# Kernel optimization log

Hardware: AMD Instinct MI355X
Metric: run time of the kernel (lower is better)

## Reference

```python
import jax, jax.numpy as jnp
import numpy as np
from jax import lax

DIM = 192
NUM_CLASSES = 4
D_INNER = 2 * DIM          # expand=2
D_STATE = 16
D_CONV = 4
DT_RANK = (DIM + 15) // 16  # ceil(192/16)=12
PATCH = 16


def _mamba_params(key, prefix):
    ks = jax.random.split(key, 9)
    s = lambda k, shape, scale: (jax.random.normal(k, shape, jnp.float32) * scale)
    p = {
        prefix + '_in_w':   s(ks[0], (2 * D_INNER, DIM), 0.02),
        prefix + '_conv_w': s(ks[1], (D_INNER, D_CONV), 0.1),
        prefix + '_conv_b': jnp.zeros((D_INNER,), jnp.float32),
        prefix + '_xproj_w': s(ks[2], (DT_RANK + 2 * D_STATE, D_INNER), 0.02),
        prefix + '_dt_w':   s(ks[3], (D_INNER, DT_RANK), 0.1),
        prefix + '_dt_b':   s(ks[4], (D_INNER,), 0.1),
        # A_log init: log(1..d_state) broadcast over d_inner (mamba default)
        prefix + '_A_log':  jnp.broadcast_to(jnp.log(jnp.arange(1, D_STATE + 1, dtype=jnp.float32)), (D_INNER, D_STATE)) + 0.0,
        prefix + '_D':      jnp.ones((D_INNER,), jnp.float32),
        prefix + '_out_w':  s(ks[5], (DIM, D_INNER), 0.02),
    }
    return p


def setup_inputs() -> dict:
    key = jax.random.key(0)
    ks = jax.random.split(key, 8)
    inp = {
        'x': jax.random.normal(ks[0], (32, 3, 384, 384), jnp.float32),
        'patch_w': jax.random.normal(ks[1], (DIM, 3, PATCH, PATCH), jnp.float32) * 0.02,
        'patch_b': jnp.zeros((DIM,), jnp.float32),
        'ln_g': jnp.ones((DIM,), jnp.float32),
        'ln_b': jnp.zeros((DIM,), jnp.float32),
        'fc_w': jax.random.normal(ks[2], (NUM_CLASSES, DIM), jnp.float32) * 0.02,
        'fc_b': jnp.zeros((NUM_CLASSES,), jnp.float32),
    }
    inp.update(_mamba_params(ks[3], 'f'))
    inp.update(_mamba_params(ks[4], 'b'))
    return inp


def _layernorm(x, g, b, eps=1e-5):
    mu = jnp.mean(x, -1, keepdims=True)
    var = jnp.mean(jnp.square(x - mu), -1, keepdims=True)
    return (x - mu) * lax.rsqrt(var + eps) * g + b


def _mamba(x, in_w, conv_w, conv_b, xproj_w, dt_w, dt_b, A_log, Dskip, out_w):
    # x: [B, L, DIM]
    Bn, L, _ = x.shape
    xz = x @ in_w.T                                    # [B, L, 2*di]
    xi, z = jnp.split(xz, 2, axis=-1)
    # causal depthwise conv1d, kernel D_CONV, left pad
    xp = jnp.pad(xi, ((0, 0), (D_CONV - 1, 0), (0, 0)))
    xc = conv_b + sum(xp[:, k:k + L, :] * conv_w[:, k] for k in range(D_CONV))
    xc = jax.nn.silu(xc)                               # [B, L, di]
    proj = xc @ xproj_w.T                              # [B, L, dtr+2*ds]
    dt, Bm, Cm = jnp.split(proj, [DT_RANK, DT_RANK + D_STATE], axis=-1)
    dt = jax.nn.softplus(dt @ dt_w.T + dt_b)           # [B, L, di]
    A = -jnp.exp(A_log)                                # [di, ds]

    def step(h, inp):
        dt_t, B_t, C_t, x_t = inp                      # [B,di],[B,ds],[B,ds],[B,di]
        dA = jnp.exp(dt_t[:, :, None] * A)             # [B, di, ds]
        h = dA * h + (dt_t * x_t)[:, :, None] * B_t[:, None, :]
        y = jnp.einsum('bds,bs->bd', h, C_t)
        return h, y

    h0 = jnp.zeros((Bn, D_INNER, D_STATE), x.dtype)
    xs = (dt.transpose(1, 0, 2), Bm.transpose(1, 0, 2),
          Cm.transpose(1, 0, 2), xc.transpose(1, 0, 2))
    _, ys = lax.scan(step, h0, xs)                     # [L, B, di]
    y = ys.transpose(1, 0, 2) + xc * Dskip
    y = y * jax.nn.silu(z)
    return y @ out_w.T                                 # [B, L, DIM]


def reference(x, patch_w, patch_b, ln_g, ln_b, fc_w, fc_b,
              f_in_w, f_conv_w, f_conv_b, f_xproj_w, f_dt_w, f_dt_b, f_A_log, f_D, f_out_w,
              b_in_w, b_conv_w, b_conv_b, b_xproj_w, b_dt_w, b_dt_b, b_A_log, b_D, b_out_w):
    Bn, C, H, W = x.shape
    Hp, Wp = H // PATCH, W // PATCH
    # patch embed: stride==kernel conv == reshape + einsum
    xr = x.reshape(Bn, C, Hp, PATCH, Wp, PATCH)
    tok = jnp.einsum('bchpwq,dcpq->bhwd', xr, patch_w) + patch_b
    tok = tok.reshape(Bn, Hp * Wp, DIM)                # [B, L, D]
    tok = _layernorm(tok, ln_g, ln_b)
    fwd = _mamba(tok, f_in_w, f_conv_w, f_conv_b, f_xproj_w, f_dt_w, f_dt_b, f_A_log, f_D, f_out_w)
    bwd = _mamba(tok[:, ::-1, :], b_in_w, b_conv_w, b_conv_b, b_xproj_w, b_dt_w, b_dt_b, b_A_log, b_D, b_out_w)
    out = fwd + bwd[:, ::-1, :]
    pooled = jnp.mean(out, axis=1)                     # adaptive avg pool to 1
    return pooled @ fc_w.T + fc_b                      # [B, num_classes]
```

## Files before the change

### kernel.cpp

```cpp
#include <hip/hip_runtime.h>
#include <hip/hip_bf16.h>

#define NC 32
#define CL 18

typedef __attribute__((ext_vector_type(8))) short short8;
typedef __attribute__((ext_vector_type(4))) float f32x4;
typedef __attribute__((ext_vector_type(2))) float f32x2;

__device__ __forceinline__ float sigm(float x){ return 1.0f/(1.0f+__expf(-x)); }

__device__ __forceinline__ ushort f2bf(float f){
  unsigned u = __float_as_uint(f);
  unsigned r = (u + 0x7fffu + ((u>>16)&1u)) >> 16;
  return (ushort)r;
}
__device__ __forceinline__ float bf2f(ushort h){ return __uint_as_float(((unsigned)h)<<16); }

__global__ __launch_bounds__(256) void k_prep_all(
    const float* __restrict__ patch_w, const float* __restrict__ f_in_w,
    const float* __restrict__ b_in_w,
    const float* __restrict__ f_xw, const float* __restrict__ b_xw,
    const float* __restrict__ f_cw, const float* __restrict__ b_cw,
    const float* __restrict__ f_al, const float* __restrict__ b_al,
    const float* __restrict__ fc_w, const float* __restrict__ f_ow,
    const float* __restrict__ b_ow,
    ushort* __restrict__ pw_h, ushort* __restrict__ pw_l,
    ushort* __restrict__ iw_h, ushort* __restrict__ iw_l,
    ushort* __restrict__ xw_h, ushort* __restrict__ xw_l,
    float* __restrict__ cwT, float* __restrict__ Abuf,
    float* __restrict__ A0fl, float* __restrict__ W2){
  const int bx = blockIdx.x, t = threadIdx.x;
  if (bx < 1728){
    int which = bx/576;
    int i = (bx - which*576)*256 + t;
    if (which==0){
      float f = patch_w[i];
      ushort hb = f2bf(f);
      pw_h[i]=hb; pw_l[i]=f2bf(f - bf2f(hb));
    } else {
      const float* src = (which==1) ? f_in_w : b_in_w;
      int dirofs = (which==1) ? 0 : 48;
      float f = src[i];
      int n = i/192, k = i%192;
      int nblk = n>>4, r = n&15, kblk = k>>5, kk = k&31;
      int lane = r + ((kk>>3)<<4), j = kk&7;
      size_t idx = ((size_t)((nblk+dirofs)*6 + kblk)*64 + lane)*8 + j;
      ushort hb = f2bf(f);
      iw_h[idx]=hb; iw_l[idx]=f2bf(f - bf2f(hb));
    }
  } else if (bx < 1872){
    int i = (bx-1728)*256 + t;
    int dir=i/(48*384), rem=i%(48*384), n=rem/384, k=rem%384;
    float v = (n<44) ? (dir?b_xw:f_xw)[n*384+k] : 0.f;
    ushort hb = f2bf(v);
    xw_h[i]=hb; xw_l[i]=f2bf(v - bf2f(hb));
  } else if (bx < 1884){
    int i = (bx-1872)*256 + t;
    int dir=i/1536, rem=i%1536, j=rem/384, k=rem%384;
    cwT[i] = (dir ? b_cw : f_cw)[k*4+j];
  } else if (bx < 1887){
    int i = (bx-1884)*256 + t;
    if (i < 768){
      int dir=i/384, di=i%384;
      const float* alp = (dir?b_al:f_al) + di*16;
      float A0 = -expf(alp[0]);
      bool fast = true;
      Abuf[(size_t)i*16] = A0;
      #pragma unroll
      for (int s=1;s<16;s++){
        float A = -expf(alp[s]);
        Abuf[(size_t)i*16+s] = A;
        fast = fast && (fabsf(A - (s+1)*A0) <= 1e-5f*(s+1)*fabsf(A0));
      }
      A0fl[i*2]=A0; A0fl[i*2+1]=fast?1.f:0.f;
    }
  } else {
    int i = (bx-1887)*256 + t;
    if (i < 768){
      int dir=i/384, di=i%384;
      const float* ow = dir ? b_ow : f_ow;
      float a0=0.f,a1=0.f,a2=0.f,a3=0.f;
      for (int d=0; d<192; ++d){
        float o = ow[d*384 + di];
        a0 += fc_w[0*192+d]*o; a1 += fc_w[1*192+d]*o;
        a2 += fc_w[2*192+d]*o; a3 += fc_w[3*192+d]*o;
      }
      W2[(0*2+dir)*384+di]=a0; W2[(1*2+dir)*384+di]=a1;
      W2[(2*2+dir)*384+di]=a2; W2[(3*2+dir)*384+di]=a3;
    }
  }
}
__device__ __forceinline__ float w2at(const float* W2, int dir, int ch, int di){
  return W2[(ch*2+dir)*384+di];
}

__global__ __launch_bounds__(1024) void k_patch(
    const float* __restrict__ x,
    const ushort* __restrict__ pw_h, const ushort* __restrict__ pw_l,
    const float* __restrict__ pb, const float* __restrict__ lng,
    const float* __restrict__ lnb,
    ushort* __restrict__ tokf_h, ushort* __restrict__ tokf_l,
    int b0, int Mc){
  __shared__ __align__(16) char sBmem[49152];
  __shared__ __align__(16) ushort sAh[64*64], sAl[64*64];
  __shared__ float sLN[4][64][2];
  ushort* sBh = (ushort*)sBmem;
  ushort* sBl = (ushort*)(sBmem + 24576);
  const int tid = threadIdx.x;
  const int m0 = blockIdx.x*64;
  const int lane = tid&63, w = tid>>6;
  const int wr = w>>2, wc = w&3;
  const int r = lane&15, g = lane>>4;
  f32x4 acc[3];
  #pragma unroll
  for (int i=0;i<3;i++) acc[i] = (f32x4){0.f,0.f,0.f,0.f};

  for (int s=0;s<12;s++){
    const int c = s>>2, p0 = (s&3)*4;
    {
      int f = tid;
      int m = f>>4, rem = f&15, pp = rem>>2, qq = rem&3;
      int rm = m0 + m;
      float4 v = make_float4(0.f,0.f,0.f,0.f);
      if (rm < Mc){
        int b = b0 + rm/576, l = rm%576, hp = l/24, wp = l%24;
        size_t idx4 = ((size_t)((b*3+c)*384) + hp*16 + p0+pp)*96 + wp*4 + qq;
        v = reinterpret_cast<const float4*>(x)[idx4];
      }
      ushort4 hv, lv;
      hv.x=f2bf(v.x); lv.x=f2bf(v.x-bf2f(hv.x));
      hv.y=f2bf(v.y); lv.y=f2bf(v.y-bf2f(hv.y));
      hv.z=f2bf(v.z); lv.z=f2bf(v.z-bf2f(hv.z));
      hv.w=f2bf(v.w); lv.w=f2bf(v.w-bf2f(hv.w));
      int byte = (m*128 + pp*32 + qq*8) ^ ((m&7)<<4);
      *reinterpret_cast<ushort4*>((char*)sAh + byte) = hv;
      *reinterpret_cast<ushort4*>((char*)sAl + byte) = lv;
    }
    #pragma unroll
    for (int i=0;i<2;i++){
      int f = tid + i*1024;
      if (f < 1536){
        int n = f>>3, k8 = f&7;
        size_t gi = (size_t)n*768 + s*64 + k8*8;
        uint4 bh = *reinterpret_cast<const uint4*>(pw_h + gi);
        uint4 bl = *reinterpret_cast<const uint4*>(pw_l + gi);
        int byte = (n*128 + k8*16) ^ ((n&7)<<4);
        *reinterpret_cast<uint4*>((char*)sBh + byte) = bh;
        *reinterpret_cast<uint4*>((char*)sBl + byte) = bl;
      }
    }
    __syncthreads();
    #pragma unroll
    for (int kk=0;kk<2;kk++){
      int arow = wr*16 + r;
      int abyte = (arow*128 + kk*64 + g*16) ^ ((arow&7)<<4);
      short8 ah = *reinterpret_cast<const short8*>((char*)sAh + abyte);
      short8 al = *reinterpret_cast<const short8*>((char*)sAl + abyte);
      #pragma unroll
      for (int nfl=0; nfl<3; nfl++){
        int brow = (wc*3+nfl)*16 + r;
        int bbyte = (brow*128 + kk*64 + g*16) ^ ((brow&7)<<4);
        short8 bh = *reinterpret_cast<const short8*>((char*)sBh + bbyte);
        short8 bll = *reinterpret_cast<const short8*>((char*)sBl + bbyte);
        acc[nfl] = __builtin_amdgcn_mfma_f32_16x16x32_bf16(ah, bh, acc[nfl], 0,0,0);
        acc[nfl] = __builtin_amdgcn_mfma_f32_16x16x32_bf16(ah, bll, acc[nfl], 0,0,0);
        acc[nfl] = __builtin_amdgcn_mfma_f32_16x16x32_bf16(al, bh, acc[nfl], 0,0,0);
      }
    }
    __syncthreads();
  }
  float pbv[3], gv[3], bv[3];
  #pragma unroll
  for (int nfl=0;nfl<3;nfl++){
    int col = (wc*3+nfl)*16 + r;
    pbv[nfl]=pb[col]; gv[nfl]=lng[col]; bv[nfl]=lnb[col];
  }
  #pragma unroll
  for (int nfl=0;nfl<3;nfl++)
    #pragma unroll
    for (int q=0;q<4;q++) acc[nfl][q] += pbv[nfl];
  float sum[4]={0,0,0,0}, sq[4]={0,0,0,0};
  #pragma unroll
  for (int nfl=0;nfl<3;nfl++)
    #pragma unroll
    for (int q=0;q<4;q++){ float v=acc[nfl][q]; sum[q]+=v; sq[q]+=v*v; }
  #pragma unroll
  for (int off=1; off<16; off<<=1){
    #pragma unroll
    for (int q=0;q<4;q++){
      sum[q]+=__shfl_xor(sum[q],off);
      sq[q] +=__shfl_xor(sq[q],off);
    }
  }
  if (r==0){
    #pragma unroll
    for (int q=0;q<4;q++){
      int row = wr*16 + g*4 + q;
      sLN[wc][row][0]=sum[q]; sLN[wc][row][1]=sq[q];
    }
  }
  __syncthreads();
  float* sT = (float*)sBmem;
  #pragma unroll
  for (int q=0;q<4;q++){
    int rl = wr*16 + g*4 + q;
    float stot = sLN[0][rl][0]+sLN[1][rl][0]+sLN[2][rl][0]+sLN[3][rl][0];
    float qtot = sLN[0][rl][1]+sLN[1][rl][1]+sLN[2][rl][1]+sLN[3][rl][1];
    float mu = stot*(1.f/192.f);
    float var = qtot*(1.f/192.f) - mu*mu;
    float rs = rsqrtf(var + 1e-5f);
    #pragma unroll
    for (int nfl=0;nfl<3;nfl++)
      sT[rl*192 + (wc*3+nfl)*16 + r] = (acc[nfl][q]-mu)*rs*gv[nfl] + bv[nfl];
  }
  __syncthreads();
  const int mB = m0>>4;
  #pragma unroll
  for (int i=0;i<2;i++){
    int fl = tid + 1024*i;
    if (fl < 1536){
      int mb = fl/384, rem = fl-mb*384, kb = rem>>6, ln = rem&63;
      int rr = ln&15, gq = ln>>4;
      const float* sp = sT + (mb*16+rr)*192 + kb*32 + gq*8;
      short8 hv, lv;
      #pragma unroll
      for (int j=0;j<8;j++){
        float v = sp[j];
        ushort hb = f2bf(v);
        hv[j] = (short)hb;
        lv[j] = (short)f2bf(v - bf2f(hb));
      }
      size_t o = ((size_t)((mB+mb)*6 + kb)*64 + ln)*8;
      *reinterpret_cast<short8*>(tokf_h + o) = hv;
      *reinterpret_cast<short8*>(tokf_l + o) = lv;
    }
  }
}

__global__ __launch_bounds__(1024) void k_inproj(
    const ushort* __restrict__ tokf_h, const ushort* __restrict__ tokf_l,
    const ushort* __restrict__ iw_h, const ushort* __restrict__ iw_l,
    float* __restrict__ xib, ushort* __restrict__ zb, int Bc, int Mc){
  __shared__ __align__(16) char sMem[65536];
  ushort* sAh = (ushort*)sMem;
  ushort* sAl = (ushort*)(sMem + 16384);
  ushort* sBh = (ushort*)(sMem + 32768);
  ushort* sBl = (ushort*)(sMem + 49152);
  const int tid = threadIdx.x;
  const int lane = tid&63, w = tid>>6;
  const int wr = w>>2, wc = w&3;
  const int r = lane&15, g = lane>>4;
  const int m0 = blockIdx.x*128;
  const int mb0 = blockIdx.x*8;
  const int nb0 = blockIdx.y*8;
  const int n0d = (blockIdx.y%6)*128;
  const bool dir1 = (blockIdx.y >= 6);
  const bool isZ = ((blockIdx.y%6) >= 3);

  f32x4 acc[2][2];
  #pragma unroll
  for (int a=0;a<2;a++)
    #pragma unroll
    for (int b=0;b<2;b++) acc[a][b] = (f32x4){0.f,0.f,0.f,0.f};

  for (int s=0;s<3;s++){
    {
      const int f = w;
      const int mf = f>>1, kk = f&1;
      const size_t ga = ((size_t)((mb0+mf)*6 + 2*s+kk)*64 + lane)*8;
      const size_t gb = ((size_t)((nb0+mf)*6 + 2*s+kk)*64 + lane)*8;
      const int so = f*512 + lane*8;
      *reinterpret_cast<short8*>(sAh+so) = *reinterpret_cast<const short8*>(tokf_h+ga);
      *reinterpret_cast<short8*>(sBh+so) = *reinterpret_cast<const short8*>(iw_h+gb);
      if (!isZ){
        *reinterpret_cast<short8*>(sAl+so) = *reinterpret_cast<const short8*>(tokf_l+ga);
        *reinterpret_cast<short8*>(sBl+so) = *reinterpret_cast<const short8*>(iw_l+gb);
      }
    }
    __syncthreads();
    #pragma unroll
    for (int kk=0;kk<2;kk++){
      short8 ah[2], al[2];
      #pragma unroll
      for (int mf=0;mf<2;mf++){
        const int fo = ((wr*2+mf)*2+kk)*512 + lane*8;
        ah[mf] = *reinterpret_cast<const short8*>(sAh+fo);
        if (!isZ) al[mf] = *reinterpret_cast<const short8*>(sAl+fo);
      }
      #pragma unroll
      for (int nf=0;nf<2;nf++){
        const int fo = ((wc*2+nf)*2+kk)*512 + lane*8;
        short8 bh = *reinterpret_cast<const short8*>(sBh+fo);
        if (isZ){
          #pragma unroll
          for (int mf=0;mf<2;mf++)
            acc[mf][nf] = __builtin_amdgcn_mfma_f32_16x16x32_bf16(ah[mf], bh, acc[mf][nf], 0,0,0);
        } else {
          short8 bl = *reinterpret_cast<const short8*>(sBl+fo);
          #pragma unroll
          for (int mf=0;mf<2;mf++){
            acc[mf][nf] = __builtin_amdgcn_mfma_f32_16x16x32_bf16(ah[mf], bh, acc[mf][nf], 0,0,0);
            acc[mf][nf] = __builtin_amdgcn_mfma_f32_16x16x32_bf16(ah[mf], bl, acc[mf][nf], 0,0,0);
            acc[mf][nf] = __builtin_amdgcn_mfma_f32_16x16x32_bf16(al[mf], bh, acc[mf][nf], 0,0,0);
          }
        }
      }
    }
    __syncthreads();
  }

  float* sT = reinterpret_cast<float*>(sMem);
  const int h_of_w = wr>>1;
  #pragma unroll
  for (int h=0; h<2; h++){
    if (h==1) __syncthreads();
    if (h_of_w == h){
      #pragma unroll
      for (int mf=0;mf<2;mf++)
        #pragma unroll
        for (int nf=0;nf<2;nf++)
          #pragma unroll
          for (int q=0;q<4;q++){
            int rl = (wr&1)*32 + mf*16 + g*4 + q;
            int c  = wc*32 + nf*16 + r;
            sT[rl*132 + c] = acc[mf][nf][q];
          }
    }
    __syncthreads();
    {
      const int rl = tid>>4, cg = tid&15;
      const int rm = m0 + h*64 + rl;
      if (rm < Mc){
        size_t row;
        if (dir1){
          int bl = rm/576, l = rm - bl*576;
          row = (size_t)(Bc + bl)*576 + (575-l);
        } else {
          row = (size_t)rm;
        }
        const float* sp = sT + rl*132 + cg*8;
        if (!isZ){
          *reinterpret_cast<f32x4*>(xib + row*384 + n0d + cg*8)     = *reinterpret_cast<const f32x4*>(sp);
          *reinterpret_cast<f32x4*>(xib + row*384 + n0d + cg*8 + 4) = *reinterpret_cast<const f32x4*>(sp+4);
        } else {
          short8 hv;
          #pragma unroll
          for (int j=0;j<8;j++){
            float v = sp[j];
            v = v*sigm(v);
            hv[j] = (short)f2bf(v);
          }
          *reinterpret_cast<short8*>(zb + row*384 + (n0d-384) + cg*8) = hv;
        }
      }
    }
  }
}

__global__ __launch_bounds__(256) void k_convx(
    const float* __restrict__ xib, const float* __restrict__ cwT,
    const float* __restrict__ f_cb, const float* __restrict__ b_cb,
    const ushort* __restrict__ xw_h, const ushort* __restrict__ xw_l,
    float* __restrict__ proj, ushort* __restrict__ xcb, int Bc){
  __shared__ __align__(16) float sRaw[67*64];
  __shared__ __align__(16) ushort sAh[64*64], sAl[64*64];
  __shared__ __align__(16) ushort sBh[48*64], sBl[48*64];
  const int dir = blockIdx.z, blk = blockIdx.y, l0 = blockIdx.x*64;
  const int tid = threadIdx.x, lane = tid&63, w = tid>>6;
  const int r = lane&15, g = lane>>4;
  const size_t seq = ((size_t)dir*Bc + blk)*576;
  const float* cwTd = cwT + dir*1536;
  const float* cbp  = dir?b_cb:f_cb;
  const ushort* bhp = xw_h + dir*48*384;
  const ushort* blp = xw_l + dir*48*384;
  f32x4 acc[3];
  #pragma unroll
  for (int i=0;i<3;i++) acc[i] = (f32x4){0.f,0.f,0.f,0.f};

  for (int kc=0; kc<6; ++kc){
    #pragma unroll
    for (int i=0;i<5;i++){
      int f = tid + i*256;
      if (f < 67*16){
        int rr = f>>4, kq = f&15;
        int l = l0 + rr - 3;
        float4 v = make_float4(0.f,0.f,0.f,0.f);
        if (l >= 0) v = *reinterpret_cast<const float4*>(xib + (seq+l)*384 + kc*64 + kq*4);
        int kqs = kq ^ (rr&15);
        *reinterpret_cast<float4*>(sRaw + rr*64 + kqs*4) = v;
      }
    }
    __syncthreads();
    #pragma unroll
    for (int i=0;i<4;i++){
      int f = tid + i*256;
      int m = f>>4, kq = f&15;
      float4 a = reinterpret_cast<const float4*>(cbp)[kc*16 + kq];
      #pragma unroll
      for (int j=0;j<4;j++){
        int rr = m + j;
        float4 rv = *reinterpret_cast<const float4*>(sRaw + rr*64 + (kq ^ (rr&15))*4);
        float4 cv = reinterpret_cast<const float4*>(cwTd)[j*96 + kc*16 + kq];
        a.x += cv.x*rv.x; a.y += cv.y*rv.y; a.z += cv.z*rv.z; a.w += cv.w*rv.w;
      }
      a.x = a.x*sigm(a.x); a.y = a.y*sigm(a.y); a.z = a.z*sigm(a.z); a.w = a.w*sigm(a.w);
      ushort4 hv, lv;
      hv.x=f2bf(a.x); lv.x=f2bf(a.x-bf2f(hv.x));
      hv.y=f2bf(a.y); lv.y=f2bf(a.y-bf2f(hv.y));
      hv.z=f2bf(a.z); lv.z=f2bf(a.z-bf2f(hv.z));
      hv.w=f2bf(a.w); lv.w=f2bf(a.w-bf2f(hv.w));
      *reinterpret_cast<ushort4*>(xcb + (seq + l0 + m)*384 + kc*64 + kq*4) = hv;
      int byte = (m*128 + kq*8) ^ ((m&7)<<4);
      *reinterpret_cast<ushort4*>((char*)sAh + byte) = hv;
      *reinterpret_cast<ushort4*>((char*)sAl + byte) = lv;
    }
    #pragma unroll
    for (int i=0;i<2;i++){
      int f = tid + i*256;
      if (f < 384){
        int n = f>>3, k8 = f&7;
        size_t gi = (size_t)n*384 + kc*64 + k8*8;
        uint4 vh = *reinterpret_cast<const uint4*>(bhp + gi);
        uint4 vl = *reinterpret_cast<const uint4*>(blp + gi);
        int byte = (n*128 + k8*16) ^ ((n&7)<<4);
        *reinterpret_cast<uint4*>((char*)sBh + byte) = vh;
        *reinterpret_cast<uint4*>((char*)sBl + byte) = vl;
      }
    }
    __syncthreads();
    #pragma unroll
    for (int kk=0;kk<2;kk++){
      int arow = w*16 + r;
      int abyte = (arow*128 + kk*64 + g*16) ^ ((arow&7)<<4);
      short8 ah = *reinterpret_cast<const short8*>((char*)sAh + abyte);
      short8 al = *reinterpret_cast<const short8*>((char*)sAl + abyte);
      #pragma unroll
      for (int nf=0;nf<3;nf++){
        int brow = nf*16 + r;
        int bbyte = (brow*128 + kk*64 + g*16) ^ ((brow&7)<<4);
        short8 bh = *reinterpret_cast<const short8*>((char*)sBh + bbyte);
        short8 bll = *reinterpret_cast<const short8*>((char*)sBl + bbyte);
        acc[nf] = __builtin_amdgcn_mfma_f32_16x16x32_bf16(ah, bh, acc[nf], 0,0,0);
        acc[nf] = __builtin_amdgcn_mfma_f32_16x16x32_bf16(ah, bll, acc[nf], 0,0,0);
        acc[nf] = __builtin_amdgcn_mfma_f32_16x16x32_bf16(al, bh, acc[nf], 0,0,0);
      }
    }
    __syncthreads();
  }
  #pragma unroll
  for (int nf=0;nf<3;nf++){
    int col = nf*16 + r;
    if (col < 44){
      #pragma unroll
      for (int q=0;q<4;q++){
        int l = l0 + w*16 + g*4 + q;
        proj[(seq+l)*44 + col] = acc[nf][q];
      }
    }
  }
}

__global__ __launch_bounds__(256) void k_scan_p1(
    const ushort* __restrict__ zb, const ushort* __restrict__ xcb,
    const float* __restrict__ proj,
    const float* __restrict__ f_dtw, const float* __restrict__ b_dtw,
    const float* __restrict__ f_dtb, const float* __restrict__ b_dtb,
    const float* __restrict__ A0fl, const float* __restrict__ Abuf,
    const float* __restrict__ f_D,  const float* __restrict__ b_D,
    const float* __restrict__ W2, float* __restrict__ dtend,
    float* __restrict__ hbuf, float* __restrict__ part, int b0, int Bc){
  const int dir=blockIdx.z, bl=blockIdx.y;
  const int gg=blockIdx.x>>3, cq=blockIdx.x&7;
  const int wv=threadIdx.x>>6, lane=threadIdx.x&63;
  const int c = cq*4 + wv;
  const int di = gg*64 + lane;
  const size_t seq = ((size_t)dir*Bc + bl)*576;
  const float* dtwp = (dir?b_dtw:f_dtw) + di*12;
  float dtw[12];
  #pragma unroll
  for (int i=0;i<3;i++){
    float4 t = reinterpret_cast<const float4*>(dtwp)[i];
    dtw[4*i]=t.x; dtw[4*i+1]=t.y; dtw[4*i+2]=t.z; dtw[4*i+3]=t.w;
  }
  float dtb = (dir?b_dtb:f_dtb)[di];
  float2 af = reinterpret_cast<const float2*>(A0fl)[dir*384+di];
  const float A0 = af.x;
  const bool fast = (af.y != 0.f);
  float A[16];
  if (!fast){
    #pragma unroll
    for (int s=0;s<16;s++) A[s] = Abuf[((size_t)dir*384+di)*16+s];
  }
  float Dv = (dir?b_D:f_D)[di];
  float w2c[4];
  #pragma unroll
  for (int ch=0;ch<4;ch++) w2c[ch] = w2at(W2,dir,ch,di);
  f32x2 h2[8];
  #pragma unroll
  for (int p=0;p<8;p++) h2[p]=(f32x2){0.f,0.f};
  float S=0.f, cum=0.f;
  const int l0 = c*CL;
  const int pbase = (int)((seq + (size_t)l0)*44);
  const ushort* xcp = xcb + di;
  const ushort* zbp2 = zb + di;
  for (int j=0;j<CL;j++){
    const size_t row = seq + l0 + j;
    const int po = __builtin_amdgcn_readfirstlane(pbase + j*44);
    const float4* pr4 = reinterpret_cast<const float4*>(proj + po);
    float4 t0=pr4[0], t1=pr4[1], t2=pr4[2];
    float dtin = dtb
      + t0.x*dtw[0]+t0.y*dtw[1]+t0.z*dtw[2]+t0.w*dtw[3]
      + t1.x*dtw[4]+t1.y*dtw[5]+t1.z*dtw[6]+t1.w*dtw[7]
      + t2.x*dtw[8]+t2.y*dtw[9]+t2.z*dtw[10]+t2.w*dtw[11];
    float dt = (dtin > 20.f) ? dtin : __logf(1.f + __expf(dtin));
    cum += dt;
    float xc = bf2f(xcp[row*384]);
    float zs = bf2f(zbp2[row*384]);
    float u = dt*xc;
    f32x2 u2 = {u,u};
    f32x2 dA2[8];
    if (fast){
      float e1=__expf(dt*A0);
      float e2=e1*e1;
      f32x2 e2v={e2,e2};
      dA2[0]=(f32x2){e1,e2};
      #pragma unroll
      for (int p=1;p<8;p++) dA2[p]=dA2[p-1]*e2v;
    } else {
      #pragma unroll
      for (int p=0;p<8;p++){
        dA2[p]=(f32x2){__expf(dt*A[2*p]), __expf(dt*A[2*p+1])};
      }
    }
    f32x2 ya={0.f,0.f}, yb={0.f,0.f};
    #pragma unroll
    for (int i=0;i<4;i++){
      float4 tb=pr4[3+i], tc=pr4[7+i];
      f32x2 B0={tb.x,tb.y}, B1={tb.z,tb.w};
      f32x2 C0={tc.x,tc.y}, C1={tc.z,tc.w};
      h2[2*i]   = dA2[2*i]*h2[2*i]     + u2*B0;
      h2[2*i+1] = dA2[2*i+1]*h2[2*i+1] + u2*B1;
      ya += h2[2*i]*C0;
      yb += h2[2*i+1]*C1;
    }
    S += ((ya[0]+ya[1])+(yb[0]+yb[1]) + xc*Dv)*zs;
  }
  dtend[(((size_t)dir*Bc + bl)*NC + c)*384 + di] = cum;
  size_t hb = ((((size_t)c*2+dir)*Bc + bl)*6 + gg)*1024;
  #pragma unroll
  for (int s=0;s<16;s++) hbuf[hb + s*64 + lane] = h2[s>>1][s&1];
  float p0=S*w2c[0], p1v=S*w2c[1], p2v=S*w2c[2], p3v=S*w2c[3];
  #pragma unroll
  for (int off=32; off>0; off>>=1){
    p0 += __shfl_xor(p0, off); p1v += __shfl_xor(p1v, off);
    p2v += __shfl_xor(p2v, off); p3v += __shfl_xor(p3v, off);
  }
  if (lane==0){
    float* dst = part + ((((size_t)dir*32 + (b0+bl))*6 + gg)*64 + c)*4;
    dst[0]=p0; dst[1]=p1v; dst[2]=p2v; dst[3]=p3v;
  }
}

__global__ __launch_bounds__(256) void k_combine(
    const float* __restrict__ dtend, float* __restrict__ hbuf,
    const float* __restrict__ A0fl, const float* __restrict__ Abuf, int Bc){
  const int gg=blockIdx.x, bl=blockIdx.y, dir=blockIdx.z;
  const int wv=threadIdx.x>>6, lane=threadIdx.x&63, di=gg*64+lane;
  float2 af = reinterpret_cast<const float2*>(A0fl)[dir*384+di];
  const bool fast = (af.y != 0.f);
  float Aeff[4];
  #pragma unroll
  for (int si=0;si<4;si++){
    int s = wv*4+si;
    Aeff[si] = fast ? af.x*(float)(s+1) : Abuf[((size_t)dir*384+di)*16+s];
  }
  float cur[4];
  size_t hx0 = ((((size_t)0*2+dir)*Bc+bl)*6+gg)*1024 + (wv*4)*64 + lane;
  #pragma unroll
  for (int si=0;si<4;si++) cur[si]=hbuf[hx0 + si*64];
  for (int c=1;c<NC;c++){
    size_t hx=((((size_t)c*2+dir)*Bc+bl)*6+gg)*1024 + (wv*4)*64 + lane;
    float tmp[4];
    #pragma unroll
    for (int si=0;si<4;si++){ tmp[si]=hbuf[hx+si*64]; hbuf[hx+si*64]=cur[si]; }
    if (c<NC-1){
      float Sdt = dtend[(((size_t)dir*Bc+bl)*NC + c)*384 + di];
      #pragma unroll
      for (int si=0;si<4;si++) cur[si] = __expf(Aeff[si]*Sdt)*cur[si] + tmp[si];
    }
  }
}

__global__ __launch_bounds__(256) void k_scan_p2(
    const ushort* __restrict__ zb, const float* __restrict__ proj,
    const float* __restrict__ hbuf,
    const float* __restrict__ f_dtw, const float* __restrict__ b_dtw,
    const float* __restrict__ f_dtb, const float* __restrict__ b_dtb,
    const float* __restrict__ A0fl, const float* __restrict__ Abuf,
    const float* __restrict__ W2, float* __restrict__ part, int b0, int Bc){
  const int dir=blockIdx.z, bl=blockIdx.y;
  const int gg=blockIdx.x>>3, cq=blockIdx.x&7;
  const int wv=threadIdx.x>>6, lane=threadIdx.x&63;
  const int c = cq*4 + wv + 1;
  const int di = gg*64 + lane;
  const size_t seq = ((size_t)dir*Bc + bl)*576;
  if (c >= NC) return;
  const float* dtwp = (dir?b_dtw:f_dtw) + di*12;
  float dtw[12];
  #pragma unroll
  for (int i=0;i<3;i++){
    float4 t = reinterpret_cast<const float4*>(dtwp)[i];
    dtw[4*i]=t.x; dtw[4*i+1]=t.y; dtw[4*i+2]=t.z; dtw[4*i+3]=t.w;
  }
  float dtb = (dir?b_dtb:f_dtb)[di];
  float2 af = reinterpret_cast<const float2*>(A0fl)[dir*384+di];
  const float A0 = af.x;
  const bool fast = (af.y != 0.f);
  float A[16];
  if (!fast){
    #pragma unroll
    for (int s=0;s<16;s++) A[s] = Abuf[((size_t)dir*384+di)*16+s];
  }
  float w2c[4];
  #pragma unroll
  for (int ch=0;ch<4;ch++) w2c[ch]=w2at(W2,dir,ch,di);
  f32x2 hh2[8];
  size_t hb=((((size_t)c*2+dir)*Bc+bl)*6+gg)*1024;
  #pragma unroll
  for (int s=0;s<16;s++) hh2[s>>1][s&1]=hbuf[hb+s*64+lane];
  float S=0.f;
  const int l0 = c*CL;
  const int pbase = (int)((seq + (size_t)l0)*44);
  const ushort* zbp2 = zb + di;
  for (int j=0;j<CL;j++){
    const size_t row = seq + l0 + j;
    const int po = __builtin_amdgcn_readfirstlane(pbase + j*44);
    const float4* pr4 = reinterpret_cast<const float4*>(proj + po);
    float4 t0=pr4[0], t1=pr4[1], t2=pr4[2];
    float dtin = dtb
      + t0.x*dtw[0]+t0.y*dtw[1]+t0.z*dtw[2]+t0.w*dtw[3]
      + t1.x*dtw[4]+t1.y*dtw[5]+t1.z*dtw[6]+t1.w*dtw[7]
      + t2.x*dtw[8]+t2.y*dtw[9]+t2.z*dtw[10]+t2.w*dtw[11];
    float dt = (dtin > 20.f) ? dtin : __logf(1.f + __expf(dtin));
    float zs = bf2f(zbp2[row*384]);
    f32x2 dA2[8];
    if (fast){
      float e1=__expf(dt*A0);
      float e2=e1*e1;
      f32x2 e2v={e2,e2};
      dA2[0]=(f32x2){e1,e2};
      #pragma unroll
      for (int p=1;p<8;p++) dA2[p]=dA2[p-1]*e2v;
    } else {
      #pragma unroll
      for (int p=0;p<8;p++){
        dA2[p]=(f32x2){__expf(dt*A[2*p]), __expf(dt*A[2*p+1])};
      }
    }
    f32x2 ya={0.f,0.f}, yb={0.f,0.f};
    #pragma unroll
    for (int i=0;i<4;i++){
      float4 tc = pr4[7+i];
      f32x2 C0={tc.x,tc.y}, C1={tc.z,tc.w};
      hh2[2*i]   = hh2[2*i]*dA2[2*i];
      hh2[2*i+1] = hh2[2*i+1]*dA2[2*i+1];
      ya += hh2[2*i]*C0;
      yb += hh2[2*i+1]*C1;
    }
    S += ((ya[0]+ya[1])+(yb[0]+yb[1]))*zs;
  }
  float p0=S*w2c[0], p1v=S*w2c[1], p2v=S*w2c[2], p3v=S*w2c[3];
  #pragma unroll
  for (int off=32; off>0; off>>=1){
    p0 += __shfl_xor(p0, off); p1v += __shfl_xor(p1v, off);
    p2v += __shfl_xor(p2v, off); p3v += __shfl_xor(p3v, off);
  }
  if (lane==0){
    float* dst = part + ((((size_t)dir*32 + (b0+bl))*6 + gg)*64 + 32 + c)*4;
    dst[0]=p0; dst[1]=p1v; dst[2]=p2v; dst[3]=p3v;
  }
}

__global__ __launch_bounds__(256) void k_final(const float* __restrict__ part,
                                               const float* __restrict__ fc_b,
                                               float* __restrict__ out){
  const int b = blockIdx.x;
  const int ch = threadIdx.x>>6, lane = threadIdx.x&63;
  float s = 0.f;
  for (int i = lane; i < 768; i += 64){
    int c = i & 63;
    if (c == 32) continue;
    int dg = i >> 6;
    int dir = dg >= 6 ? 1 : 0;
    int g = dg - dir*6;
    s += part[((((size_t)dir*32 + b)*6 + g)*64 + c)*4 + ch];
  }
  #pragma unroll
  for (int off=32; off>0; off>>=1) s += __shfl_xor(s, off);
  if (lane==0) out[b*4+ch] = fc_b[ch] + s*(1.0f/576.0f);
}

extern "C" void kernel_launch(void* const* d_in, const int* in_sizes, int n_in,
                              void* d_out, int out_size, void* d_ws, size_t ws_size,
                              hipStream_t stream){
  const float* x       = (const float*)d_in[0];
  const float* patch_w = (const float*)d_in[1];
  const float* patch_b = (const float*)d_in[2];
  const float* ln_g    = (const float*)d_in[3];
  const float* ln_b    = (const float*)d_in[4];
  const float* fc_w    = (const float*)d_in[5];
  const float* fc_b    = (const float*)d_in[6];
  const float* f_in_w  = (const float*)d_in[7];
  const float* f_cw    = (const float*)d_in[8];
  const float* f_cb    = (const float*)d_in[9];
  const float* f_xw    = (const float*)d_in[10];
  const float* f_dtw   = (const float*)d_in[11];
  const float* f_dtb   = (const float*)d_in[12];
  const float* f_al    = (const float*)d_in[13];
  const float* f_D     = (const float*)d_in[14];
  const float* f_ow    = (const float*)d_in[15];
  const float* b_in_w  = (const float*)d_in[16];
  const float* b_cw    = (const float*)d_in[17];
  const float* b_cb    = (const float*)d_in[18];
  const float* b_xw    = (const float*)d_in[19];
  const float* b_dtw   = (const float*)d_in[20];
  const float* b_dtb   = (const float*)d_in[21];
  const float* b_al    = (const float*)d_in[22];
  const float* b_D     = (const float*)d_in[23];
  const float* b_ow    = (const float*)d_in[24];
  float* out = (float*)d_out;
  float* ws  = (float*)d_ws;

  float* W2    = ws;
  float* part  = W2 + 3072;
  ushort* pw_h = (ushort*)(part + 98304);
  ushort* pw_l = pw_h + 147456;
  ushort* iw_h = pw_l + 147456;
  ushort* iw_l = iw_h + 294912;
  ushort* xw_h = iw_l + 294912;
  ushort* xw_l = xw_h + 36864;
  float* cwT   = (float*)(xw_l + 36864);
  float* Abuf  = cwT + 3072;
  float* A0fl  = Abuf + 12288;
  float* base  = A0fl + 1536;

  const size_t FIXED = 3072 + 98304 + 2*73728 + 2*147456 + 2*18432 + 3072
                     + 12288 + 1536;
  const size_t perB = 110592ull + 442368ull + 110592ull + 110592ull
                    + 24576ull + 393216ull;
  int Bc = 32;
  while (Bc > 1 && (FIXED + (size_t)Bc*perB)*4ull > ws_size) Bc >>= 1;

  ushort* tokf_h = (ushort*)base;
  ushort* tokf_l = tokf_h + (size_t)Bc*110592ull;
  float* prj  = base;
  float* xib  = base + (size_t)Bc*110592ull;
  ushort* zbp = (ushort*)(xib + (size_t)Bc*442368ull);
  ushort* xcb = zbp + (size_t)Bc*442368ull;
  float* dtnd = (float*)(xcb + (size_t)Bc*442368ull);
  float* hbf  = dtnd + (size_t)Bc*24576ull;

  k_prep_all<<<dim3(1890),dim3(256),0,stream>>>(patch_w, f_in_w, b_in_w,
                                                f_xw, b_xw, f_cw, b_cw,
                                                f_al, b_al, fc_w, f_ow, b_ow,
                                                pw_h, pw_l, iw_h, iw_l,
                                                xw_h, xw_l, cwT, Abuf, A0fl, W2);

  for (int b0=0; b0<32; b0+=Bc){
    const int Mc = Bc*576;
    k_patch<<<dim3((Mc+63)/64),dim3(1024),0,stream>>>(x, pw_h, pw_l, patch_b,
                                                      ln_g, ln_b, tokf_h, tokf_l, b0, Mc);
    k_inproj<<<dim3((Mc+127)/128,12),dim3(1024),0,stream>>>(tokf_h, tokf_l, iw_h, iw_l,
                                                            xib, zbp, Bc, Mc);
    k_convx<<<dim3(9,Bc,2),dim3(256),0,stream>>>(xib, cwT, f_cb, b_cb,
                                                 xw_h, xw_l, prj, xcb, Bc);
    k_scan_p1<<<dim3(48,Bc,2),dim3(256),0,stream>>>(zbp, xcb, prj,
                                                    f_dtw,b_dtw, f_dtb,b_dtb,
                                                    A0fl, Abuf, f_D,b_D,
                                                    W2, dtnd, hbf, part, b0, Bc);
    k_combine<<<dim3(6,Bc,2),dim3(256),0,stream>>>(dtnd, hbf, A0fl, Abuf, Bc);
    k_scan_p2<<<dim3(48,Bc,2),dim3(256),0,stream>>>(zbp, prj, hbf,
                                                    f_dtw,b_dtw, f_dtb,b_dtb,
                                                    A0fl, Abuf, W2, part, b0, Bc);
  }
  k_final<<<dim3(32),dim3(256),0,stream>>>(part, fc_b, out);
}
```

Before: 238.2 us.

## Process two d_inner channels per thread in scan and combine kernels

Result: faster. 228.5 us (-4.1%).

```diff
diff --git a/kernel.cpp b/kernel.cpp
--- a/kernel.cpp
+++ b/kernel.cpp
@@ -461,6 +461,20 @@
   }
 }
 
+__device__ __forceinline__ void build_dA2_fast(float e1, f32x2 dA2[8]){
+  float e2 = e1*e1;
+  f32x2 d0 = {e1, e2};
+  float e4 = e2*e2;
+  f32x2 e2v = {e2,e2}, e4v = {e4,e4};
+  f32x2 d1 = d0*e2v;
+  f32x2 d2 = d0*e4v;
+  f32x2 d3 = d1*e4v;
+  float e8 = e4*e4;
+  f32x2 e8v = {e8,e8};
+  dA2[0]=d0; dA2[1]=d1; dA2[2]=d2; dA2[3]=d3;
+  dA2[4]=d0*e8v; dA2[5]=d1*e8v; dA2[6]=d2*e8v; dA2[7]=d3*e8v;
+}
+
 __global__ __launch_bounds__(256) void k_scan_p1(
     const ushort* __restrict__ zb, const ushort* __restrict__ xcb,
     const float* __restrict__ proj,
@@ -474,90 +488,107 @@
   const int gg=blockIdx.x>>3, cq=blockIdx.x&7;
   const int wv=threadIdx.x>>6, lane=threadIdx.x&63;
   const int c = cq*4 + wv;
-  const int di = gg*64 + lane;
+  const int di0 = gg*128 + lane*2;
   const size_t seq = ((size_t)dir*Bc + bl)*576;
-  const float* dtwp = (dir?b_dtw:f_dtw) + di*12;
-  float dtw[12];
-  #pragma unroll
-  for (int i=0;i<3;i++){
-    float4 t = reinterpret_cast<const float4*>(dtwp)[i];
-    dtw[4*i]=t.x; dtw[4*i+1]=t.y; dtw[4*i+2]=t.z; dtw[4*i+3]=t.w;
-  }
-  float dtb = (dir?b_dtb:f_dtb)[di];
-  float2 af = reinterpret_cast<const float2*>(A0fl)[dir*384+di];
-  const float A0 = af.x;
-  const bool fast = (af.y != 0.f);
-  float A[16];
-  if (!fast){
-    #pragma unroll
-    for (int s=0;s<16;s++) A[s] = Abuf[((size_t)dir*384+di)*16+s];
-  }
-  float Dv = (dir?b_D:f_D)[di];
-  float w2c[4];
-  #pragma unroll
-  for (int ch=0;ch<4;ch++) w2c[ch] = w2at(W2,dir,ch,di);
-  f32x2 h2[8];
-  #pragma unroll
-  for (int p=0;p<8;p++) h2[p]=(f32x2){0.f,0.f};
-  float S=0.f, cum=0.f;
+  const float* dtwp = (dir?b_dtw:f_dtw) + (size_t)di0*12;
+  f32x2 dtw2[12];
+  {
+    const float4* dp = reinterpret_cast<const float4*>(dtwp);
+    #pragma unroll
+    for (int i=0;i<3;i++){
+      float4 fa = dp[i], fb = dp[i+3];
+      dtw2[4*i+0] = (f32x2){fa.x, fb.x};
+      dtw2[4*i+1] = (f32x2){fa.y, fb.y};
+      dtw2[4*i+2] = (f32x2){fa.z, fb.z};
+      dtw2[4*i+3] = (f32x2){fa.w, fb.w};
+    }
+  }
+  float2 dtb2 = *reinterpret_cast<const float2*>((dir?b_dtb:f_dtb)+di0);
+  float4 af = *reinterpret_cast<const float4*>(A0fl + ((size_t)dir*384+di0)*2);
+  const float A0a = af.x, A0b = af.z;
+  const bool fast = (af.y != 0.f) && (af.w != 0.f);
+  const float* Abp = Abuf + ((size_t)dir*384+di0)*16;
+  float2 Dv2 = *reinterpret_cast<const float2*>((dir?b_D:f_D)+di0);
+  float2 w2c2[4];
+  #pragma unroll
+  for (int ch=0;ch<4;ch++)
+    w2c2[ch] = *reinterpret_cast<const float2*>(W2 + (ch*2+dir)*384 + di0);
+  f32x2 h2a[8], h2b[8];
+  #pragma unroll
+  for (int p=0;p<8;p++){ h2a[p]=(f32x2){0.f,0.f}; h2b[p]=(f32x2){0.f,0.f}; }
+  float Sa=0.f, Sb=0.f, cuma=0.f, cumb=0.f;
   const int l0 = c*CL;
   const int pbase = (int)((seq + (size_t)l0)*44);
-  const ushort* xcp = xcb + di;
-  const ushort* zbp2 = zb + di;
+  const ushort* xcp = xcb + di0;
+  const ushort* zbp2 = zb + di0;
   for (int j=0;j<CL;j++){
     const size_t row = seq + l0 + j;
     const int po = __builtin_amdgcn_readfirstlane(pbase + j*44);
     const float4* pr4 = reinterpret_cast<const float4*>(proj + po);
     float4 t0=pr4[0], t1=pr4[1], t2=pr4[2];
-    float dtin = dtb
-      + t0.x*dtw[0]+t0.y*dtw[1]+t0.z*dtw[2]+t0.w*dtw[3]
-      + t1.x*dtw[4]+t1.y*dtw[5]+t1.z*dtw[6]+t1.w*dtw[7]
-      + t2.x*dtw[8]+t2.y*dtw[9]+t2.z*dtw[10]+t2.w*dtw[11];
-    float dt = (dtin > 20.f) ? dtin : __logf(1.f + __expf(dtin));
-    cum += dt;
-    float xc = bf2f(xcp[row*384]);
-    float zs = bf2f(zbp2[row*384]);
-    float u = dt*xc;
-    f32x2 u2 = {u,u};
-    f32x2 dA2[8];
+    f32x2 dtin2 = (f32x2){dtb2.x, dtb2.y};
+    dtin2 += (f32x2){t0.x,t0.x}*dtw2[0]; dtin2 += (f32x2){t0.y,t0.y}*dtw2[1];
+    dtin2 += (f32x2){t0.z,t0.z}*dtw2[2]; dtin2 += (f32x2){t0.w,t0.w}*dtw2[3];
+    dtin2 += (f32x2){t1.x,t1.x}*dtw2[4]; dtin2 += (f32x2){t1.y,t1.y}*dtw2[5];
+    dtin2 += (f32x2){t1.z,t1.z}*dtw2[6]; dtin2 += (f32x2){t1.w,t1.w}*dtw2[7];
+    dtin2 += (f32x2){t2.x,t2.x}*dtw2[8]; dtin2 += (f32x2){t2.y,t2.y}*dtw2[9];
+    dtin2 += (f32x2){t2.z,t2.z}*dtw2[10]; dtin2 += (f32x2){t2.w,t2.w}*dtw2[11];
+    float dta = (dtin2[0] > 20.f) ? dtin2[0] : __logf(1.f + __expf(dtin2[0]));
+    float dtb_ = (dtin2[1] > 20.f) ? dtin2[1] : __logf(1.f + __expf(dtin2[1]));
+    cuma += dta; cumb += dtb_;
+    uint xu = *reinterpret_cast<const uint*>(xcp + row*384);
+    uint zu = *reinterpret_cast<const uint*>(zbp2 + row*384);
+    float xca = bf2f((ushort)(xu&0xffffu)), xcbv = bf2f((ushort)(xu>>16));
+    float zsa = bf2f((ushort)(zu&0xffffu)), zsb = bf2f((ushort)(zu>>16));
+    float ua = dta*xca, ub = dtb_*xcbv;
+    f32x2 u2a = {ua,ua}, u2b = {ub,ub};
+    f32x2 dA2a[8], dA2b[8];
     if (fast){
-      float e1=__expf(dt*A0);
-      float e2=e1*e1;
-      f32x2 e2v={e2,e2};
-      dA2[0]=(f32x2){e1,e2};
-      #pragma unroll
-      for (int p=1;p<8;p++) dA2[p]=dA2[p-1]*e2v;
+      build_dA2_fast(__expf(dta*A0a), dA2a);
+      build_dA2_fast(__expf(dtb_*A0b), dA2b);
     } else {
       #pragma unroll
       for (int p=0;p<8;p++){
-        dA2[p]=(f32x2){__expf(dt*A[2*p]), __expf(dt*A[2*p+1])};
-      }
-    }
-    f32x2 ya={0.f,0.f}, yb={0.f,0.f};
+        dA2a[p]=(f32x2){__expf(dta*Abp[2*p]), __expf(dta*Abp[2*p+1])};
+        dA2b[p]=(f32x2){__expf(dtb_*Abp[16+2*p]), __expf(dtb_*Abp[16+2*p+1])};
+      }
+    }
+    f32x2 yaa={0.f,0.f}, yba={0.f,0.f}, yab={0.f,0.f}, ybb={0.f,0.f};
     #pragma unroll
     for (int i=0;i<4;i++){
-      float4 tb=pr4[3+i], tc=pr4[7+i];
-      f32x2 B0={tb.x,tb.y}, B1={tb.z,tb.w};
-      f32x2 C0={tc.x,tc.y}, C1={tc.z,tc.w};
-      h2[2*i]   = dA2[2*i]*h2[2*i]     + u2*B0;
-      h2[2*i+1] = dA2[2*i+1]*h2[2*i+1] + u2*B1;
-      ya += h2[2*i]*C0;
-      yb += h2[2*i+1]*C1;
-    }
-    S += ((ya[0]+ya[1])+(yb[0]+yb[1]) + xc*Dv)*zs;
-  }
-  dtend[(((size_t)dir*Bc + bl)*NC + c)*384 + di] = cum;
-  size_t hb = ((((size_t)c*2+dir)*Bc + bl)*6 + gg)*1024;
-  #pragma unroll
-  for (int s=0;s<16;s++) hbuf[hb + s*64 + lane] = h2[s>>1][s&1];
-  float p0=S*w2c[0], p1v=S*w2c[1], p2v=S*w2c[2], p3v=S*w2c[3];
+      float4 tb4=pr4[3+i], tc4=pr4[7+i];
+      f32x2 B0={tb4.x,tb4.y}, B1={tb4.z,tb4.w};
+      f32x2 C0={tc4.x,tc4.y}, C1={tc4.z,tc4.w};
+      h2a[2*i]   = dA2a[2*i]*h2a[2*i]     + u2a*B0;
+      h2a[2*i+1] = dA2a[2*i+1]*h2a[2*i+1] + u2a*B1;
+      yaa += h2a[2*i]*C0;
+      yba += h2a[2*i+1]*C1;
+      h2b[2*i]   = dA2b[2*i]*h2b[2*i]     + u2b*B0;
+      h2b[2*i+1] = dA2b[2*i+1]*h2b[2*i+1] + u2b*B1;
+      yab += h2b[2*i]*C0;
+      ybb += h2b[2*i+1]*C1;
+    }
+    Sa += ((yaa[0]+yaa[1])+(yba[0]+yba[1]) + xca*Dv2.x)*zsa;
+    Sb += ((yab[0]+yab[1])+(ybb[0]+ybb[1]) + xcbv*Dv2.y)*zsb;
+  }
+  *reinterpret_cast<float2*>(dtend + ((((size_t)dir*Bc + bl)*NC + c)*384 + di0))
+      = make_float2(cuma, cumb);
+  size_t hb = ((((size_t)c*2+dir)*Bc + bl)*3 + gg)*2048;
+  #pragma unroll
+  for (int s=0;s<16;s++)
+    *reinterpret_cast<float2*>(hbuf + hb + s*128 + lane*2)
+        = make_float2(h2a[s>>1][s&1], h2b[s>>1][s&1]);
+  float p0 = Sa*w2c2[0].x + Sb*w2c2[0].y;
+  float p1v= Sa*w2c2[1].x + Sb*w2c2[1].y;
+  float p2v= Sa*w2c2[2].x + Sb*w2c2[2].y;
+  float p3v= Sa*w2c2[3].x + Sb*w2c2[3].y;
   #pragma unroll
   for (int off=32; off>0; off>>=1){
     p0 += __shfl_xor(p0, off); p1v += __shfl_xor(p1v, off);
     p2v += __shfl_xor(p2v, off); p3v += __shfl_xor(p3v, off);
   }
   if (lane==0){
-    float* dst = part + ((((size_t)dir*32 + (b0+bl))*6 + gg)*64 + c)*4;
+    float* dst = part + ((((size_t)dir*32 + (b0+bl))*3 + gg)*64 + c)*4;
     dst[0]=p0; dst[1]=p1v; dst[2]=p2v; dst[3]=p3v;
   }
 }
@@ -566,28 +597,37 @@
     const float* __restrict__ dtend, float* __restrict__ hbuf,
     const float* __restrict__ A0fl, const float* __restrict__ Abuf, int Bc){
   const int gg=blockIdx.x, bl=blockIdx.y, dir=blockIdx.z;
-  const int wv=threadIdx.x>>6, lane=threadIdx.x&63, di=gg*64+lane;
-  float2 af = reinterpret_cast<const float2*>(A0fl)[dir*384+di];
-  const bool fast = (af.y != 0.f);
-  float Aeff[4];
+  const int wv=threadIdx.x>>6, lane=threadIdx.x&63;
+  const int di0=gg*128+lane*2;
+  float4 af = *reinterpret_cast<const float4*>(A0fl + ((size_t)dir*384+di0)*2);
+  const bool fast = (af.y != 0.f) && (af.w != 0.f);
+  const float* Abp = Abuf + ((size_t)dir*384+di0)*16;
+  float Aa[4], Ab[4];
   #pragma unroll
   for (int si=0;si<4;si++){
     int s = wv*4+si;
-    Aeff[si] = fast ? af.x*(float)(s+1) : Abuf[((size_t)dir*384+di)*16+s];
-  }
-  float cur[4];
-  size_t hx0 = ((((size_t)0*2+dir)*Bc+bl)*6+gg)*1024 + (wv*4)*64 + lane;
-  #pragma unroll
-  for (int si=0;si<4;si++) cur[si]=hbuf[hx0 + si*64];
+    Aa[si] = fast ? af.x*(float)(s+1) : Abp[s];
+    Ab[si] = fast ? af.z*(float)(s+1) : Abp[16+s];
+  }
+  float2 cur[4];
+  size_t hx0 = ((((size_t)(0*2+dir)*Bc+bl)*3+gg)*2048) + (wv*4)*128 + lane*2;
+  #pragma unroll
+  for (int si=0;si<4;si++) cur[si]=*reinterpret_cast<float2*>(hbuf + hx0 + si*128);
   for (int c=1;c<NC;c++){
-    size_t hx=((((size_t)c*2+dir)*Bc+bl)*6+gg)*1024 + (wv*4)*64 + lane;
-    float tmp[4];
-    #pragma unroll
-    for (int si=0;si<4;si++){ tmp[si]=hbuf[hx+si*64]; hbuf[hx+si*64]=cur[si]; }
+    size_t hx=((((size_t)c*2+dir)*Bc+bl)*3+gg)*2048 + (wv*4)*128 + lane*2;
+    float2 tmp[4];
+    #pragma unroll
+    for (int si=0;si<4;si++){
+      tmp[si]=*reinterpret_cast<float2*>(hbuf+hx+si*128);
+      *reinterpret_cast<float2*>(hbuf+hx+si*128)=cur[si];
+    }
     if (c<NC-1){
-      float Sdt = dtend[(((size_t)dir*Bc+bl)*NC + c)*384 + di];
-      #pragma unroll
-      for (int si=0;si<4;si++) cur[si] = __expf(Aeff[si]*Sdt)*cur[si] + tmp[si];
+      float2 Sdt = *reinterpret_cast<const float2*>(dtend + ((((size_t)dir*Bc+bl)*NC + c)*384 + di0));
+      #pragma unroll
+      for (int si=0;si<4;si++){
+        cur[si].x = __expf(Aa[si]*Sdt.x)*cur[si].x + tmp[si].x;
+        cur[si].y = __expf(Ab[si]*Sdt.y)*cur[si].y + tmp[si].y;
+      }
     }
   }
 }
@@ -603,81 +643,97 @@
   const int gg=blockIdx.x>>3, cq=blockIdx.x&7;
   const int wv=threadIdx.x>>6, lane=threadIdx.x&63;
   const int c = cq*4 + wv + 1;
-  const int di = gg*64 + lane;
+  const int di0 = gg*128 + lane*2;
   const size_t seq = ((size_t)dir*Bc + bl)*576;
   if (c >= NC) return;
-  const float* dtwp = (dir?b_dtw:f_dtw) + di*12;
-  float dtw[12];
-  #pragma unroll
-  for (int i=0;i<3;i++){
-    float4 t = reinterpret_cast<const float4*>(dtwp)[i];
-    dtw[4*i]=t.x; dtw[4*i+1]=t.y; dtw[4*i+2]=t.z; dtw[4*i+3]=t.w;
-  }
-  float dtb = (dir?b_dtb:f_dtb)[di];
-  float2 af = reinterpret_cast<const float2*>(A0fl)[dir*384+di];
-  const float A0 = af.x;
-  const bool fast = (af.y != 0.f);
-  float A[16];
-  if (!fast){
-    #pragma unroll
-    for (int s=0;s<16;s++) A[s] = Abuf[((size_t)dir*384+di)*16+s];
-  }
-  float w2c[4];
-  #pragma unroll
-  for (int ch=0;ch<4;ch++) w2c[ch]=w2at(W2,dir,ch,di);
-  f32x2 hh2[8];
-  size_t hb=((((size_t)c*2+dir)*Bc+bl)*6+gg)*1024;
-  #pragma unroll
-  for (int s=0;s<16;s++) hh2[s>>1][s&1]=hbuf[hb+s*64+lane];
-  float S=0.f;
+  const float* dtwp = (dir?b_dtw:f_dtw) + (size_t)di0*12;
+  f32x2 dtw2[12];
+  {
+    const float4* dp = reinterpret_cast<const float4*>(dtwp);
+    #pragma unroll
+    for (int i=0;i<3;i++){
+      float4 fa = dp[i], fb = dp[i+3];
+      dtw2[4*i+0] = (f32x2){fa.x, fb.x};
+      dtw2[4*i+1] = (f32x2){fa.y, fb.y};
+      dtw2[4*i+2] = (f32x2){fa.z, fb.z};
+      dtw2[4*i+3] = (f32x2){fa.w, fb.w};
+    }
+  }
+  float2 dtb2 = *reinterpret_cast<const float2*>((dir?b_dtb:f_dtb)+di0);
+  float4 af = *reinterpret_cast<const float4*>(A0fl + ((size_t)dir*384+di0)*2);
+  const float A0a = af.x, A0b = af.z;
+  const bool fast = (af.y != 0.f) && (af.w != 0.f);
+  const float* Abp = Abuf + ((size_t)dir*384+di0)*16;
+  float2 w2c2[4];
+  #pragma unroll
+  for (int ch=0;ch<4;ch++)
+    w2c2[ch] = *reinterpret_cast<const float2*>(W2 + (ch*2+dir)*384 + di0);
+  f32x2 hh2a[8], hh2b[8];
+  size_t hb=((((size_t)c*2+dir)*Bc+bl)*3+gg)*2048;
+  #pragma unroll
+  for (int s=0;s<16;s++){
+    float2 v = *reinterpret_cast<const float2*>(hbuf + hb + s*128 + lane*2);
+    hh2a[s>>1][s&1]=v.x; hh2b[s>>1][s&1]=v.y;
+  }
+  float Sa=0.f, Sb=0.f;
   const int l0 = c*CL;
   const int pbase = (int)((seq + (size_t)l0)*44);
-  const ushort* zbp2 = zb + di;
+  const ushort* zbp2 = zb + di0;
   for (int j=0;j<CL;j++){
     const size_t row = seq + l0 + j;
     const int po = __builtin_amdgcn_readfirstlane(pbase + j*44);
     const float4* pr4 = reinterpret_cast<const float4*>(proj + po);
     float4 t0=pr4[0], t1=pr4[1], t2=pr4[2];
-    float dtin = dtb
-      + t0.x*dtw[0]+t0.y*dtw[1]+t0.z*dtw[2]+t0.w*dtw[3]
-      + t1.x*dtw[4]+t1.y*dtw[5]+t1.z*dtw[6]+t1.w*dtw[7]
-      + t2.x*dtw[8]+t2.y*dtw[9]+t2.z*dtw[10]+t2.w*dtw[11];
-    float dt = (dtin > 20.f) ? dtin : __logf(1.f + __expf(dtin));
-    float zs = bf2f(zbp2[row*384]);
-    f32x2 dA2[8];
+    f32x2 dtin2 = (f32x2){dtb2.x, dtb2.y};
+    dtin2 += (f32x2){t0.x,t0.x}*dtw2[0]; dtin2 += (f32x2){t0.y,t0.y}*dtw2[1];
+    dtin2 += (f32x2){t0.z,t0.z}*dtw2[2]; dtin2 += (f32x2){t0.w,t0.w}*dtw2[3];
+    dtin2 += (f32x2){t1.x,t1.x}*dtw2[4]; dtin2 += (f32x2){t1.y,t1.y}*dtw2[5];
+    dtin2 += (f32x2){t1.z,t1.z}*dtw2[6]; dtin2 += (f32x2){t1.w,t1.w}*dtw2[7];
+    dtin2 += (f32x2){t2.x,t2.x}*dtw2[8]; dtin2 += (f32x2){t2.y,t2.y}*dtw2[9];
+    dtin2 += (f32x2){t2.z,t2.z}*dtw2[10]; dtin2 += (f32x2){t2.w,t2.w}*dtw2[11];
+    float dta = (dtin2[0] > 20.f) ? dtin2[0] : __logf(1.f + __expf(dtin2[0]));
+    float dtb_ = (dtin2[1] > 20.f) ? dtin2[1] : __logf(1.f + __expf(dtin2[1]));
+    uint zu = *reinterpret_cast<const uint*>(zbp2 + row*384);
+    float zsa = bf2f((ushort)(zu&0xffffu)), zsb = bf2f((ushort)(zu>>16));
+    f32x2 dA2a[8], dA2b[8];
     if (fast){
-      float e1=__expf(dt*A0);
-      float e2=e1*e1;
-      f32x2 e2v={e2,e2};
-      dA2[0]=(f32x2){e1,e2};
-      #pragma unroll
-      for (int p=1;p<8;p++) dA2[p]=dA2[p-1]*e2v;
+      build_dA2_fast(__expf(dta*A0a), dA2a);
+      build_dA2_fast(__expf(dtb_*A0b), dA2b);
     } else {
       #pragma unroll
       for (int p=0;p<8;p++){
-        dA2[p]=(f32x2){__expf(dt*A[2*p]), __expf(dt*A[2*p+1])};
-      }
-    }
-    f32x2 ya={0.f,0.f}, yb={0.f,0.f};
+        dA2a[p]=(f32x2){__expf(dta*Abp[2*p]), __expf(dta*Abp[2*p+1])};
+        dA2b[p]=(f32x2){__expf(dtb_*Abp[16+2*p]), __expf(dtb_*Abp[16+2*p+1])};
+      }
+    }
+    f32x2 yaa={0.f,0.f}, yba={0.f,0.f}, yab={0.f,0.f}, ybb={0.f,0.f};
     #pragma unroll
     for (int i=0;i<4;i++){
-      float4 tc = pr4[7+i];
-      f32x2 C0={tc.x,tc.y}, C1={tc.z,tc.w};
-      hh2[2*i]   = hh2[2*i]*dA2[2*i];
-      hh2[2*i+1] = hh2[2*i+1]*dA2[2*i+1];
-      ya += hh2[2*i]*C0;
-      yb += hh2[2*i+1]*C1;
-    }
-    S += ((ya[0]+ya[1])+(yb[0]+yb[1]))*zs;
-  }
-  float p0=S*w2c[0], p1v=S*w2c[1], p2v=S*w2c[2], p3v=S*w2c[3];
+      float4 tc4 = pr4[7+i];
+      f32x2 C0={tc4.x,tc4.y}, C1={tc4.z,tc4.w};
+      hh2a[2*i]   = hh2a[2*i]*dA2a[2*i];
+      hh2a[2*i+1] = hh2a[2*i+1]*dA2a[2*i+1];
+      yaa += hh2a[2*i]*C0;
+      yba += hh2a[2*i+1]*C1;
+      hh2b[2*i]   = hh2b[2*i]*dA2b[2*i];
+      hh2b[2*i+1] = hh2b[2*i+1]*dA2b[2*i+1];
+      yab += hh2b[2*i]*C0;
+      ybb += hh2b[2*i+1]*C1;
+    }
+    Sa += ((yaa[0]+yaa[1])+(yba[0]+yba[1]))*zsa;
+    Sb += ((yab[0]+yab[1])+(ybb[0]+ybb[1]))*zsb;
+  }
+  float p0 = Sa*w2c2[0].x + Sb*w2c2[0].y;
+  float p1v= Sa*w2c2[1].x + Sb*w2c2[1].y;
+  float p2v= Sa*w2c2[2].x + Sb*w2c2[2].y;
+  float p3v= Sa*w2c2[3].x + Sb*w2c2[3].y;
   #pragma unroll
   for (int off=32; off>0; off>>=1){
     p0 += __shfl_xor(p0, off); p1v += __shfl_xor(p1v, off);
     p2v += __shfl_xor(p2v, off); p3v += __shfl_xor(p3v, off);
   }
   if (lane==0){
-    float* dst = part + ((((size_t)dir*32 + (b0+bl))*6 + gg)*64 + 32 + c)*4;
+    float* dst = part + ((((size_t)dir*32 + (b0+bl))*3 + gg)*64 + 32 + c)*4;
     dst[0]=p0; dst[1]=p1v; dst[2]=p2v; dst[3]=p3v;
   }
 }
@@ -688,13 +744,13 @@
   const int b = blockIdx.x;
   const int ch = threadIdx.x>>6, lane = threadIdx.x&63;
   float s = 0.f;
-  for (int i = lane; i < 768; i += 64){
+  for (int i = lane; i < 384; i += 64){
     int c = i & 63;
     if (c == 32) continue;
     int dg = i >> 6;
-    int dir = dg >= 6 ? 1 : 0;
-    int g = dg - dir*6;
-    s += part[((((size_t)dir*32 + b)*6 + g)*64 + c)*4 + ch];
+    int dir = dg >= 3 ? 1 : 0;
+    int g = dg - dir*3;
+    s += part[((((size_t)dir*32 + b)*3 + g)*64 + c)*4 + ch];
   }
   #pragma unroll
   for (int off=32; off>0; off>>=1) s += __shfl_xor(s, off);
@@ -775,12 +831,12 @@
                                                             xib, zbp, Bc, Mc);
     k_convx<<<dim3(9,Bc,2),dim3(256),0,stream>>>(xib, cwT, f_cb, b_cb,
                                                  xw_h, xw_l, prj, xcb, Bc);
-    k_scan_p1<<<dim3(48,Bc,2),dim3(256),0,stream>>>(zbp, xcb, prj,
+    k_scan_p1<<<dim3(24,Bc,2),dim3(256),0,stream>>>(zbp, xcb, prj,
                                                     f_dtw,b_dtw, f_dtb,b_dtb,
                                                     A0fl, Abuf, f_D,b_D,
                                                     W2, dtnd, hbf, part, b0, Bc);
-    k_combine<<<dim3(6,Bc,2),dim3(256),0,stream>>>(dtnd, hbf, A0fl, Abuf, Bc);
-    k_scan_p2<<<dim3(48,Bc,2),dim3(256),0,stream>>>(zbp, prj, hbf,
+    k_combine<<<dim3(3,Bc,2),dim3(256),0,stream>>>(dtnd, hbf, A0fl, Abuf, Bc);
+    k_scan_p2<<<dim3(24,Bc,2),dim3(256),0,stream>>>(zbp, prj, hbf,
                                                     f_dtw,b_dtw, f_dtb,b_dtb,
                                                     A0fl, Abuf, W2, part, b0, Bc);
   }
```
